# Performance work log

Measured on AMD Instinct MI355X. Metric: run time of the kernel, lower is better.

The kernel has to match this reference:

```python
import jax, jax.numpy as jnp
import numpy as np

N_NODES = 100000
N_EDGES = 1000000
N_GRAPHS = 256
NUM_NODE_TYPES = 200
EMB_DIM = 64
HID_DIM = 32


def _gcn_conv(x, src, dst, W, b, n):
    """PyG GCNConv: x' = D^-1/2 (A+I) D^-1/2 (x W) + b. src/dst already include self-loops."""
    xw = x @ W  # [n, out]
    ones = jnp.ones(dst.shape, dtype=xw.dtype)
    deg = jax.ops.segment_sum(ones, dst, num_segments=n)  # in-degree incl. self-loop
    dinv = jnp.where(deg > 0, jax.lax.rsqrt(jnp.maximum(deg, 1e-12)), 0.0)
    norm = dinv[src] * dinv[dst]  # [E+n]
    msg = xw[src] * norm[:, None]  # gather + scale
    return jax.ops.segment_sum(msg, dst, num_segments=n) + b


def setup_inputs() -> dict:
    key = jax.random.key(0)
    ks = jax.random.split(key, 12)
    x = jax.random.randint(ks[0], (N_NODES, 1), 0, NUM_NODE_TYPES, dtype=jnp.int64)
    edge_index = jax.random.randint(ks[1], (2, N_EDGES), 0, N_NODES, dtype=jnp.int64)
    batch = jnp.sort(jax.random.randint(ks[2], (N_NODES,), 0, N_GRAPHS, dtype=jnp.int64))
    s = 0.05
    emb = jax.random.normal(ks[3], (NUM_NODE_TYPES, EMB_DIM), dtype=jnp.float32)
    W1 = jax.random.normal(ks[4], (EMB_DIM, HID_DIM), dtype=jnp.float32) * s
    b1 = jnp.zeros((HID_DIM,), dtype=jnp.float32)
    W2 = jax.random.normal(ks[5], (HID_DIM, HID_DIM), dtype=jnp.float32) * s
    b2 = jnp.zeros((HID_DIM,), dtype=jnp.float32)
    Wc1 = jax.random.normal(ks[6], (HID_DIM, 16), dtype=jnp.float32) * s
    bc1 = jnp.zeros((16,), dtype=jnp.float32)
    Wc2 = jax.random.normal(ks[7], (16, 1), dtype=jnp.float32) * s
    bc2 = jnp.zeros((1,), dtype=jnp.float32)
    return dict(x=x, edge_index=edge_index, batch=batch, emb=emb, W1=W1, b1=b1,
                W2=W2, b2=b2, Wc1=Wc1, bc1=bc1, Wc2=Wc2, bc2=bc2)


def reference(x, edge_index, batch, emb, W1, b1, W2, b2, Wc1, bc1, Wc2, bc2):
    n = x.shape[0]
    ids = x[:, 0]  # x.squeeze()
    loops = jnp.arange(n, dtype=edge_index.dtype)
    src = jnp.concatenate([edge_index[0], loops])
    dst = jnp.concatenate([edge_index[1], loops])

    h = emb[ids]  # [N, 64] embedding lookup
    h = jax.nn.relu(_gcn_conv(h, src, dst, W1, b1, n))
    h = jax.nn.relu(_gcn_conv(h, src, dst, W2, b2, n))

    # global_mean_pool over batch segments
    seg_sum = jax.ops.segment_sum(h, batch, num_segments=N_GRAPHS)
    counts = jax.ops.segment_sum(jnp.ones((n,), dtype=h.dtype), batch, num_segments=N_GRAPHS)
    pooled = seg_sum / jnp.maximum(counts, 1.0)[:, None]  # [B, 32]

    hc = jax.nn.relu(pooled @ Wc1 + bc1)
    return jax.nn.sigmoid(hc @ Wc2 + bc2)  # [B, 1]
```

## Files before the change

kernel.cpp:

```cpp
#include <hip/hip_runtime.h>
#include <hip/hip_fp16.h>
#include <math.h>

#define N_NODES   100000
#define N_EDGES   1000000
#define N_GRAPHS  256
#define NUM_TYPES 200
#define EMB       64
#define HID       32
#define BSHIFT    8
#define BSTRIDE   256
#define NBUCK     391
#define EPB       4096
#define NCHUNK    245
#define MAXBE     4096
#define SRCBITS   17
#define SRCMASK   0x1FFFF


__global__ __launch_bounds__(256) void k_binA(const int* __restrict__ dst,
                                              int* __restrict__ counts) {
    __shared__ int cnt[NBUCK];
    int tid = threadIdx.x, k = blockIdx.x;
    for (int b = tid; b < NBUCK; b += 256) cnt[b] = 0;
    __syncthreads();
    int base = k * EPB;
    int n = min(EPB, N_EDGES - base);
    for (int t = tid; t < n; t += 256) atomicAdd(&cnt[dst[base + t] >> BSHIFT], 1);
    __syncthreads();
    for (int b = tid; b < NBUCK; b += 256) counts[k * NBUCK + b] = cnt[b];
}

__global__ __launch_bounds__(512) void k_misc(const int* __restrict__ counts,
                                              int* __restrict__ offs,
                                              int* __restrict__ bbase,
                                              const float* __restrict__ emb,
                                              const float* __restrict__ W1,
                                              float* __restrict__ table,
                                              float* __restrict__ pooled) {
    int tid = threadIdx.x;
    if (blockIdx.x == 0) {
        __shared__ int sA[512], sB[512];
        int total = 0;
        if (tid < NBUCK)
            for (int k = 0; k < NCHUNK; ++k) total += counts[k * NBUCK + tid];
        sA[tid] = (tid < NBUCK) ? total : 0;
        __syncthreads();
        int* in = sA; int* ot = sB;
        for (int off = 1; off < 512; off <<= 1) {
            ot[tid] = in[tid] + (tid >= off ? in[tid - off] : 0);
            __syncthreads();
            int* tmp = in; in = ot; ot = tmp;
        }
        int excl = in[tid] - ((tid < NBUCK) ? total : 0);
        if (tid < NBUCK) {
            bbase[tid] = excl;
            int run = excl;
            for (int k = 0; k < NCHUNK; ++k) {
                offs[k * NBUCK + tid] = run;
                run += counts[k * NBUCK + tid];
            }
        }
        if (tid == 0) bbase[NBUCK] = N_EDGES;
    } else if (blockIdx.x == 1) {
        for (int t = tid; t < NUM_TYPES * HID; t += 512) {
            int ty = t / HID, j = t % HID;
            float s = 0.f;
            for (int k = 0; k < EMB; ++k) s = fmaf(emb[ty * EMB + k], W1[k * HID + j], s);
            table[t] = s;
        }
    } else {
        for (int t = tid; t < N_GRAPHS * HID; t += 512) pooled[t] = 0.f;
    }
}

__global__ __launch_bounds__(512) void k_binB(const int* __restrict__ src,
                                              const int* __restrict__ dst,
                                              const int* __restrict__ offs,
                                              int* __restrict__ binned) {
    __shared__ int srcl[EPB];
    __shared__ int dstl[EPB];
    __shared__ unsigned short rank16[EPB];
    __shared__ unsigned short perm[EPB];
    __shared__ int cnt[NBUCK];
    __shared__ int loc[NBUCK];
    __shared__ int offsL[NBUCK];
    __shared__ int sA[512], sB[512];
    int tid = threadIdx.x, k = blockIdx.x;
    int base = k * EPB;
    int n = min(EPB, N_EDGES - base);
    if (tid < NBUCK) { cnt[tid] = 0; offsL[tid] = offs[k * NBUCK + tid]; }
    __syncthreads();
    for (int t = tid; t < n; t += 512) {
        int s = src[base + t], d = dst[base + t];
        srcl[t] = s; dstl[t] = d;
        rank16[t] = (unsigned short)atomicAdd(&cnt[d >> BSHIFT], 1);
    }
    __syncthreads();
    sA[tid] = (tid < NBUCK) ? cnt[tid] : 0;
    __syncthreads();
    int* in = sA; int* ot = sB;
    for (int off = 1; off < 512; off <<= 1) {
        ot[tid] = in[tid] + (tid >= off ? in[tid - off] : 0);
        __syncthreads();
        int* tmp = in; in = ot; ot = tmp;
    }
    if (tid < NBUCK) loc[tid] = in[tid] - cnt[tid];
    __syncthreads();
    for (int t = tid; t < n; t += 512) {
        int b = dstl[t] >> BSHIFT;
        perm[loc[b] + rank16[t]] = (unsigned short)t;
    }
    __syncthreads();
    for (int t = tid; t < n; t += 512) {
        int e = perm[t];
        int d = dstl[e], b = d >> BSHIFT;
        int gpos = offsL[b] + (t - loc[b]);
        binned[gpos] = ((d & (BSTRIDE - 1)) << SRCBITS) | srcl[e];
    }
}

__global__ __launch_bounds__(512) void k_csr(const int* __restrict__ binned,
                                             const int* __restrict__ bbase,
                                             const int* __restrict__ ids,
                                             int* __restrict__ ssrc,
                                             int* __restrict__ row_ptr,
                                             float* __restrict__ dinv,
                                             int2* __restrict__ nodeinfo) {
    __shared__ int pk[MAXBE];
    __shared__ unsigned char dl[MAXBE];
    __shared__ unsigned short rank16[MAXBE];
    __shared__ unsigned short perm[MAXBE];
    __shared__ int degL[BSTRIDE];
    __shared__ int loc[BSTRIDE];
    __shared__ int sA[BSTRIDE], sB[BSTRIDE];
    int tid = threadIdx.x, b = blockIdx.x;
    int e0 = bbase[b], e1 = bbase[b + 1];
    int n = min(e1 - e0, MAXBE);
    if (tid < BSTRIDE) degL[tid] = 0;
    __syncthreads();
    for (int t = tid; t < n; t += 512) {
        int v = binned[e0 + t];
        pk[t] = v;
        int d = v >> SRCBITS;
        dl[t] = (unsigned char)d;
        rank16[t] = (unsigned short)atomicAdd(&degL[d], 1);
    }
    __syncthreads();
    if (tid < BSTRIDE) sA[tid] = degL[tid];
    __syncthreads();
    int* in = sA; int* ot = sB;
    for (int off = 1; off < BSTRIDE; off <<= 1) {
        if (tid < BSTRIDE) ot[tid] = in[tid] + (tid >= off ? in[tid - off] : 0);
        __syncthreads();
        int* tmp = in; in = ot; ot = tmp;
    }
    if (tid < BSTRIDE) loc[tid] = in[tid] - degL[tid];
    __syncthreads();
    for (int t = tid; t < n; t += 512)
        perm[loc[dl[t]] + rank16[t]] = (unsigned short)t;
    __syncthreads();
    for (int t = tid; t < n; t += 512)
        ssrc[e0 + t] = pk[perm[t]] & SRCMASK;
    if (tid < BSTRIDE) {
        int i = b * BSTRIDE + tid;
        if (i < N_NODES) {
            row_ptr[i] = e0 + loc[tid];
            float dv = rsqrtf((float)degL[tid] + 1.0f);
            dinv[i] = dv;
            nodeinfo[i] = make_int2(ids[i], __float_as_int(dv));
        }
    }
    if (b == NBUCK - 1 && tid == 0) row_ptr[N_NODES] = N_EDGES;
}

__global__ __launch_bounds__(256) void k_einfo(const int* __restrict__ ssrc,
                                               const int2* __restrict__ nodeinfo,
                                               unsigned int* __restrict__ einfo) {
    int e0 = (blockIdx.x * 256 + threadIdx.x) * 4;
    if (e0 >= N_EDGES) return;
    int4 s4 = *(const int4*)(ssrc + e0);
    int2 n0 = nodeinfo[s4.x], n1 = nodeinfo[s4.y];
    int2 n2 = nodeinfo[s4.z], n3 = nodeinfo[s4.w];
    uint4 r;
    r.x = ((unsigned)n0.x << 16) | __half_as_ushort(__float2half(__int_as_float(n0.y)));
    r.y = ((unsigned)n1.x << 16) | __half_as_ushort(__float2half(__int_as_float(n1.y)));
    r.z = ((unsigned)n2.x << 16) | __half_as_ushort(__float2half(__int_as_float(n2.y)));
    r.w = ((unsigned)n3.x << 16) | __half_as_ushort(__float2half(__int_as_float(n3.y)));
    *(uint4*)(einfo + e0) = r;
}


__global__ __launch_bounds__(256) void k_gather1(
        const int2* __restrict__ nodeinfo, const float* __restrict__ table,
        const int* __restrict__ row_ptr, const unsigned int* __restrict__ einfo,
        const float* __restrict__ b1, const float* __restrict__ W2,
        uint2* __restrict__ Y2h) {
    __shared__ float w[HID * HID];
    for (int k = threadIdx.x; k < HID * HID; k += 256) w[k] = W2[k];
    __syncthreads();

    int t = blockIdx.x * 256 + threadIdx.x;
    int i = t >> 3, p = t & 7;
    const float4* tab4 = (const float4*)table;

    int s0 = row_ptr[i], n = row_ptr[i + 1] - s0;
    int2 self = nodeinfo[i];
    float di = __int_as_float(self.y);
    float4 acc = tab4[self.x * 8 + p];
    acc.x *= di; acc.y *= di; acc.z *= di; acc.w *= di;

    for (int e = 0; e < n; e += 8) {
        unsigned int ei[8];
#pragma unroll
        for (int u = 0; u < 8; ++u) {
            int idx = e + u; idx = (idx > n - 1) ? n - 1 : idx;
            ei[u] = einfo[s0 + idx];
        }
#pragma unroll
        for (int u = 0; u < 8; ++u) {
            float ds = (e + u < n)
                ? __half2float(__ushort_as_half((unsigned short)(ei[u] & 0xFFFF))) : 0.f;
            float4 v = tab4[(ei[u] >> 16) * 8 + p];
            acc.x = fmaf(v.x, ds, acc.x);
            acc.y = fmaf(v.y, ds, acc.y);
            acc.z = fmaf(v.z, ds, acc.z);
            acc.w = fmaf(v.w, ds, acc.w);
        }
    }
    float4 bb = ((const float4*)b1)[p];
    float4 h;
    h.x = fmaxf(fmaf(di, acc.x, bb.x), 0.f);
    h.y = fmaxf(fmaf(di, acc.y, bb.y), 0.f);
    h.z = fmaxf(fmaf(di, acc.z, bb.z), 0.f);
    h.w = fmaxf(fmaf(di, acc.w, bb.w), 0.f);

    float o0 = 0.f, o1 = 0.f, o2 = 0.f, o3 = 0.f;
    const float4* w4 = (const float4*)w;
#pragma unroll
    for (int q = 0; q < 8; ++q) {
        float4 hq;
        hq.x = __shfl(h.x, q, 8);
        hq.y = __shfl(h.y, q, 8);
        hq.z = __shfl(h.z, q, 8);
        hq.w = __shfl(h.w, q, 8);
        float4 w0 = w4[(4 * q + 0) * 8 + p];
        float4 w1 = w4[(4 * q + 1) * 8 + p];
        float4 w2 = w4[(4 * q + 2) * 8 + p];
        float4 w3 = w4[(4 * q + 3) * 8 + p];
        o0 = fmaf(hq.x, w0.x, o0); o1 = fmaf(hq.x, w0.y, o1); o2 = fmaf(hq.x, w0.z, o2); o3 = fmaf(hq.x, w0.w, o3);
        o0 = fmaf(hq.y, w1.x, o0); o1 = fmaf(hq.y, w1.y, o1); o2 = fmaf(hq.y, w1.z, o2); o3 = fmaf(hq.y, w1.w, o3);
        o0 = fmaf(hq.z, w2.x, o0); o1 = fmaf(hq.z, w2.y, o1); o2 = fmaf(hq.z, w2.z, o2); o3 = fmaf(hq.z, w2.w, o3);
        o0 = fmaf(hq.w, w3.x, o0); o1 = fmaf(hq.w, w3.y, o1); o2 = fmaf(hq.w, w3.z, o2); o3 = fmaf(hq.w, w3.w, o3);
    }
    __half2 h01 = __halves2half2(__float2half(o0 * di), __float2half(o1 * di));
    __half2 h23 = __halves2half2(__float2half(o2 * di), __float2half(o3 * di));
    uint2 wv;
    wv.x = *(unsigned int*)&h01;
    wv.y = *(unsigned int*)&h23;
    Y2h[i * 8 + p] = wv;
}

__global__ __launch_bounds__(256) void k_gather2(
        const uint2* __restrict__ Y2h, const int* __restrict__ row_ptr,
        const int* __restrict__ ssrc, const float* __restrict__ dinv,
        const float* __restrict__ b2, const int* __restrict__ batch,
        float* __restrict__ pooled) {
    __shared__ float lp[32][HID];
    for (int k = threadIdx.x; k < 32 * HID; k += 256) ((float*)lp)[k] = 0.f;
    __syncthreads();

    int t = blockIdx.x * 256 + threadIdx.x;
    int i = t >> 3, p = t & 7;
    int i0 = (blockIdx.x * 256) >> 3;
    int gFirst = batch[i0];

    uint2 selfv = Y2h[i * 8 + p];
    float2 sa = __half22float2(*(__half2*)&selfv.x);
    float2 sb = __half22float2(*(__half2*)&selfv.y);
    float4 acc = make_float4(sa.x, sa.y, sb.x, sb.y);

    int s0 = row_ptr[i], n = row_ptr[i + 1] - s0;
    for (int e = 0; e < n; e += 8) {
        int ss[8];
#pragma unroll
        for (int u = 0; u < 8; ++u) {
            int idx = e + u; idx = (idx > n - 1) ? n - 1 : idx;
            ss[u] = ssrc[s0 + idx];
        }
        uint2 v[8];
#pragma unroll
        for (int u = 0; u < 8; ++u) v[u] = Y2h[ss[u] * 8 + p];
#pragma unroll
        for (int u = 0; u < 8; ++u) {
            float wg = (e + u < n) ? 1.f : 0.f;
            float2 fa = __half22float2(*(__half2*)&v[u].x);
            float2 fb = __half22float2(*(__half2*)&v[u].y);
            acc.x = fmaf(fa.x, wg, acc.x);
            acc.y = fmaf(fa.y, wg, acc.y);
            acc.z = fmaf(fb.x, wg, acc.z);
            acc.w = fmaf(fb.y, wg, acc.w);
        }
    }
    float di = dinv[i];
    float4 bb = ((const float4*)b2)[p];
    float4 h;
    h.x = fmaxf(fmaf(di, acc.x, bb.x), 0.f);
    h.y = fmaxf(fmaf(di, acc.y, bb.y), 0.f);
    h.z = fmaxf(fmaf(di, acc.z, bb.z), 0.f);
    h.w = fmaxf(fmaf(di, acc.w, bb.w), 0.f);

    int gl = batch[i] - gFirst;
    atomicAdd(&lp[gl][p * 4 + 0], h.x);
    atomicAdd(&lp[gl][p * 4 + 1], h.y);
    atomicAdd(&lp[gl][p * 4 + 2], h.z);
    atomicAdd(&lp[gl][p * 4 + 3], h.w);
    __syncthreads();

    int gLast = batch[i0 + 31];
    int ng = gLast - gFirst + 1;
    for (int k = threadIdx.x; k < ng * HID; k += 256) {
        float v = lp[k / HID][k % HID];
        if (v != 0.f) atomicAdd(&pooled[(gFirst + k / HID) * HID + (k % HID)], v);
    }
}

__global__ void k_head(const float* __restrict__ pooled, const int* __restrict__ batch,
                       const float* __restrict__ Wc1, const float* __restrict__ bc1,
                       const float* __restrict__ Wc2, const float* __restrict__ bc2,
                       float* __restrict__ out) {
    int g = blockIdx.x * blockDim.x + threadIdx.x;
    if (g >= N_GRAPHS) return;
    int lo = 0, hi = N_NODES;
    while (lo < hi) { int mid = (lo + hi) >> 1; if (batch[mid] < g) lo = mid + 1; else hi = mid; }
    int start = lo;
    hi = N_NODES;
    while (lo < hi) { int mid = (lo + hi) >> 1; if (batch[mid] < g + 1) lo = mid + 1; else hi = mid; }
    int end = lo;
    float inv = 1.0f / fmaxf((float)(end - start), 1.0f);
    float m[HID];
    for (int j = 0; j < HID; ++j) m[j] = pooled[g * HID + j] * inv;
    float hc[16];
    for (int j = 0; j < 16; ++j) {
        float s = bc1[j];
        for (int k = 0; k < HID; ++k) s = fmaf(m[k], Wc1[k * 16 + j], s);
        hc[j] = fmaxf(s, 0.f);
    }
    float s = bc2[0];
    for (int k = 0; k < 16; ++k) s = fmaf(hc[k], Wc2[k], s);
    out[g] = 1.0f / (1.0f + expf(-s));
}


extern "C" void kernel_launch(void* const* d_in, const int* in_sizes, int n_in,
                              void* d_out, int out_size, void* d_ws, size_t ws_size,
                              hipStream_t stream) {
    const int*   ids  = (const int*)d_in[0];
    const int*   src  = (const int*)d_in[1];
    const int*   dst  = ((const int*)d_in[1]) + N_EDGES;
    const int*   batch = (const int*)d_in[2];
    const float* emb  = (const float*)d_in[3];
    const float* W1   = (const float*)d_in[4];
    const float* b1   = (const float*)d_in[5];
    const float* W2   = (const float*)d_in[6];
    const float* b2   = (const float*)d_in[7];
    const float* Wc1  = (const float*)d_in[8];
    const float* bc1  = (const float*)d_in[9];
    const float* Wc2  = (const float*)d_in[10];
    const float* bc2  = (const float*)d_in[11];
    float* out = (float*)d_out;

    int* W = (int*)d_ws;
    size_t o = 0;
    uint2* Y2h      = (uint2*)(W + o);        o += 1600000;
    int*   binned   = W + o;                  o += N_EDGES;
    int*   ssrc     = W + o;                  o += N_EDGES;
    unsigned int* einfo = (unsigned int*)(W + o); o += N_EDGES;
    int2*  nodeinfo = (int2*)(W + o);         o += 2 * N_NODES;
    int*   counts   = W + o;                  o += NCHUNK * NBUCK;
    int*   offs     = W + o;                  o += NCHUNK * NBUCK;
    int*   bbase    = W + o;                  o += NBUCK + 1;
    int*   row_ptr  = W + o;                  o += N_NODES + 1;
    o = (o + 3) & ~(size_t)3;
    float* dinv     = (float*)(W + o);        o += N_NODES;
    float* table    = (float*)(W + o);        o += NUM_TYPES * HID;
    float* pooled   = (float*)(W + o);

    const int B = 256;
    const int gNode8 = (N_NODES * 8) / B;

    k_binA<<<NCHUNK, B, 0, stream>>>(dst, counts);
    k_misc<<<3, 512, 0, stream>>>(counts, offs, bbase, emb, W1, table, pooled);
    k_binB<<<NCHUNK, 512, 0, stream>>>(src, dst, offs, binned);
    k_csr<<<NBUCK, 512, 0, stream>>>(binned, bbase, ids, ssrc, row_ptr, dinv, nodeinfo);
    k_einfo<<<(N_EDGES / 4 + B - 1) / B, B, 0, stream>>>(ssrc, nodeinfo, einfo);

    k_gather1<<<gNode8, B, 0, stream>>>(nodeinfo, table, row_ptr, einfo, b1, W2, Y2h);
    k_gather2<<<gNode8, B, 0, stream>>>((const uint2*)Y2h, row_ptr, ssrc, dinv, b2,
                                        batch, pooled);
    k_head<<<1, N_GRAPHS, 0, stream>>>(pooled, batch, Wc1, bc1, Wc2, bc2, out);
}
```

Measured before the change: 120.6 us.

## Fuse edge-info packing into first gather kernel via shared-memory staging

Removes the separate k_einfo kernel and its 4MB global einfo array. Each gather1 block now reads the ssrc and nodeinfo entries for its 32 nodes' edges, packs them (type id and half-precision dinv) into a 1024-entry shared buffer, and the per-node loops read from LDS. A fallback path reads global memory directly if a block's edge count exceeds the buffer. This saves a launch and a global write/read round trip, at the cost of extra per-block staging work and a barrier.

```diff
diff --git a/kernel.cpp b/kernel.cpp
--- a/kernel.cpp
+++ b/kernel.cpp
@@ -16,6 +16,7 @@
 #define MAXBE     4096
 #define SRCBITS   17
 #define SRCMASK   0x1FFFF
+#define ELOC      1024
 
 
 __global__ __launch_bounds__(256) void k_binA(const int* __restrict__ dst,
@@ -174,54 +175,68 @@
     if (b == NBUCK - 1 && tid == 0) row_ptr[N_NODES] = N_EDGES;
 }
 
-__global__ __launch_bounds__(256) void k_einfo(const int* __restrict__ ssrc,
-                                               const int2* __restrict__ nodeinfo,
-                                               unsigned int* __restrict__ einfo) {
-    int e0 = (blockIdx.x * 256 + threadIdx.x) * 4;
-    if (e0 >= N_EDGES) return;
-    int4 s4 = *(const int4*)(ssrc + e0);
-    int2 n0 = nodeinfo[s4.x], n1 = nodeinfo[s4.y];
-    int2 n2 = nodeinfo[s4.z], n3 = nodeinfo[s4.w];
-    uint4 r;
-    r.x = ((unsigned)n0.x << 16) | __half_as_ushort(__float2half(__int_as_float(n0.y)));
-    r.y = ((unsigned)n1.x << 16) | __half_as_ushort(__float2half(__int_as_float(n1.y)));
-    r.z = ((unsigned)n2.x << 16) | __half_as_ushort(__float2half(__int_as_float(n2.y)));
-    r.w = ((unsigned)n3.x << 16) | __half_as_ushort(__float2half(__int_as_float(n3.y)));
-    *(uint4*)(einfo + e0) = r;
-}
-
 
 __global__ __launch_bounds__(256) void k_gather1(
         const int2* __restrict__ nodeinfo, const float* __restrict__ table,
-        const int* __restrict__ row_ptr, const unsigned int* __restrict__ einfo,
+        const int* __restrict__ row_ptr, const int* __restrict__ ssrc,
         const float* __restrict__ b1, const float* __restrict__ W2,
         uint2* __restrict__ Y2h) {
     __shared__ float w[HID * HID];
-    for (int k = threadIdx.x; k < HID * HID; k += 256) w[k] = W2[k];
-    __syncthreads();
-
-    int t = blockIdx.x * 256 + threadIdx.x;
+    __shared__ unsigned int eloc[ELOC];
+    int tid = threadIdx.x;
+    for (int k = tid; k < HID * HID; k += 256) w[k] = W2[k];
+
+    int i0 = (blockIdx.x * 256) >> 3;
+    int eb0 = row_ptr[i0];
+    int eb1 = row_ptr[i0 + 32];
+    int ne = eb1 - eb0;
+    bool fits = (ne <= ELOC);
+    if (fits) {
+        for (int t = tid; t < ne; t += 256) {
+            int s = ssrc[eb0 + t];
+            int2 ni = nodeinfo[s];
+            eloc[t] = ((unsigned)ni.x << 16) |
+                      __half_as_ushort(__float2half(__int_as_float(ni.y)));
+        }
+    }
+    __syncthreads();
+
+    int t = blockIdx.x * 256 + tid;
     int i = t >> 3, p = t & 7;
     const float4* tab4 = (const float4*)table;
 
     int s0 = row_ptr[i], n = row_ptr[i + 1] - s0;
+    int l0 = s0 - eb0;
     int2 self = nodeinfo[i];
     float di = __int_as_float(self.y);
     float4 acc = tab4[self.x * 8 + p];
     acc.x *= di; acc.y *= di; acc.z *= di; acc.w *= di;
 
-    for (int e = 0; e < n; e += 8) {
-        unsigned int ei[8];
-#pragma unroll
-        for (int u = 0; u < 8; ++u) {
-            int idx = e + u; idx = (idx > n - 1) ? n - 1 : idx;
-            ei[u] = einfo[s0 + idx];
-        }
-#pragma unroll
-        for (int u = 0; u < 8; ++u) {
-            float ds = (e + u < n)
-                ? __half2float(__ushort_as_half((unsigned short)(ei[u] & 0xFFFF))) : 0.f;
-            float4 v = tab4[(ei[u] >> 16) * 8 + p];
+    if (fits) {
+        for (int e = 0; e < n; e += 8) {
+            unsigned int ei[8];
+#pragma unroll
+            for (int u = 0; u < 8; ++u) {
+                int idx = e + u; idx = (idx > n - 1) ? n - 1 : idx;
+                ei[u] = eloc[l0 + idx];
+            }
+#pragma unroll
+            for (int u = 0; u < 8; ++u) {
+                float ds = (e + u < n)
+                    ? __half2float(__ushort_as_half((unsigned short)(ei[u] & 0xFFFF))) : 0.f;
+                float4 v = tab4[(ei[u] >> 16) * 8 + p];
+                acc.x = fmaf(v.x, ds, acc.x);
+                acc.y = fmaf(v.y, ds, acc.y);
+                acc.z = fmaf(v.z, ds, acc.z);
+                acc.w = fmaf(v.w, ds, acc.w);
+            }
+        }
+    } else {
+        for (int e = 0; e < n; ++e) {
+            int s = ssrc[s0 + e];
+            int2 ni = nodeinfo[s];
+            float ds = __half2float(__float2half(__int_as_float(ni.y)));
+            float4 v = tab4[ni.x * 8 + p];
             acc.x = fmaf(v.x, ds, acc.x);
             acc.y = fmaf(v.y, ds, acc.y);
             acc.z = fmaf(v.z, ds, acc.z);
@@ -375,7 +390,6 @@
     uint2* Y2h      = (uint2*)(W + o);        o += 1600000;
     int*   binned   = W + o;                  o += N_EDGES;
     int*   ssrc     = W + o;                  o += N_EDGES;
-    unsigned int* einfo = (unsigned int*)(W + o); o += N_EDGES;
     int2*  nodeinfo = (int2*)(W + o);         o += 2 * N_NODES;
     int*   counts   = W + o;                  o += NCHUNK * NBUCK;
     int*   offs     = W + o;                  o += NCHUNK * NBUCK;
@@ -393,9 +407,8 @@
     k_misc<<<3, 512, 0, stream>>>(counts, offs, bbase, emb, W1, table, pooled);
     k_binB<<<NCHUNK, 512, 0, stream>>>(src, dst, offs, binned);
     k_csr<<<NBUCK, 512, 0, stream>>>(binned, bbase, ids, ssrc, row_ptr, dinv, nodeinfo);
-    k_einfo<<<(N_EDGES / 4 + B - 1) / B, B, 0, stream>>>(ssrc, nodeinfo, einfo);
-
-    k_gather1<<<gNode8, B, 0, stream>>>(nodeinfo, table, row_ptr, einfo, b1, W2, Y2h);
+
+    k_gather1<<<gNode8, B, 0, stream>>>(nodeinfo, table, row_ptr, ssrc, b1, W2, Y2h);
     k_gather2<<<gNode8, B, 0, stream>>>((const uint2*)Y2h, row_ptr, ssrc, dinv, b2,
                                         batch, pooled);
     k_head<<<1, N_GRAPHS, 0, stream>>>(pooled, batch, Wc1, bc1, Wc2, bc2, out);
```

Result: faster. 117.9 us (-2.2%).
